# Kernel optimization log

Measured on AMD Instinct MI355X. Metric: run time of the kernel, lower is better.

## Reference

```python
import jax, jax.numpy as jnp
import numpy as np

HEADS = 8
DIM_HEAD = 64


def setup_inputs() -> dict:
    key = jax.random.key(0)
    k1, k2, k3 = jax.random.split(key, 3)
    b, hw, n, dim = 2, 1024, 64, 512
    x = jax.random.normal(k1, (b, hw, n, dim), dtype=jnp.float32)
    w_qkv = jax.random.normal(k2, (3 * HEADS * DIM_HEAD, dim), dtype=jnp.float32) * 0.02
    pos_bias = jax.random.normal(k3, (HEADS, n, n), dtype=jnp.float32)
    # one batch attends everywhere, one focuses on the present frame (eye mask)
    focus_present_mask = jnp.arange(b).astype(bool)
    return {"x": x, "w_qkv": w_qkv, "pos_bias": pos_bias,
            "focus_present_mask": focus_present_mask}


def reference(x, w_qkv, pos_bias, focus_present_mask):
    b, hw, n, dim = x.shape
    h, d = HEADS, DIM_HEAD
    scale = d ** -0.5

    # fused qkv projection (no bias)
    qkv = jnp.einsum('bsnc,ec->bsne', x, w_qkv)          # (b, hw, n, 3*h*d)
    q, k, v = jnp.split(qkv, 3, axis=-1)

    def to_heads(t):  # '... n (h d) -> ... h n d'
        return jnp.moveaxis(t.reshape(b, hw, n, h, d), 3, 2)

    q, k, v = map(to_heads, (q, k, v))                   # (b, hw, h, n, d)
    q = q * scale

    sim = jnp.einsum('bshid,bshjd->bshij', q, k)         # (b, hw, h, n, n)
    sim = sim + pos_bias                                 # broadcast (h, n, n)

    # focus-present mask: eye for focused batches, all-ones otherwise
    eye = jnp.eye(n, dtype=bool)
    ones = jnp.ones((n, n), dtype=bool)
    mask = jnp.where(focus_present_mask[:, None, None, None, None],
                     eye[None, None, None], ones[None, None, None])  # (b,1,1,n,n)
    neg_max = -jnp.finfo(sim.dtype).max
    sim = jnp.where(mask, sim, neg_max)

    attn = jax.nn.softmax(sim, axis=-1)                  # includes the amax shift
    out = jnp.einsum('bshij,bshjd->bshid', attn, v)      # (b, hw, h, n, d)
    out = jnp.moveaxis(out, 2, 3).reshape(b, hw, n, h * d)  # '... h n d -> ... n (h d)'
    return out
```

## Files before the change

### kernel.cpp

```cpp
#include <hip/hip_runtime.h>
#include <hip/hip_bf16.h>


typedef __attribute__((ext_vector_type(4))) float f32x4;
typedef __attribute__((ext_vector_type(8))) short s16x8;

#define DIM 512

__device__ __forceinline__ short f2bf(float f) {
    unsigned int u = __builtin_bit_cast(unsigned int, f);
    u += 0x7fffu + ((u >> 16) & 1u);
    return (short)(u >> 16);
}
__device__ __forceinline__ f32x4 ntld4(const float* p) {
    return __builtin_nontemporal_load((const f32x4*)p);
}
__device__ __forceinline__ void ntst4(float* p, f32x4 v) {
    __builtin_nontemporal_store(v, (f32x4*)p);
}
__device__ __forceinline__ s16x8 pack8(f32x4 a, f32x4 b) {
    s16x8 v;
    v[0] = f2bf(a[0]); v[1] = f2bf(a[1]); v[2] = f2bf(a[2]); v[3] = f2bf(a[3]);
    v[4] = f2bf(b[0]); v[5] = f2bf(b[1]); v[6] = f2bf(b[2]); v[7] = f2bf(b[3]);
    return v;
}
__device__ __forceinline__ int xaddr(int row, int kb) {
    return (row << 10) + (kb ^ ((row & 7) << 4));
}
__device__ __forceinline__ int taddr(int row, int kb) {
    return (row << 7) + (kb ^ ((row & 7) << 4));
}

__global__ void conv_w(const float* __restrict__ w, unsigned short* __restrict__ wb) {
    int gid  = blockIdx.x * 256 + threadIdx.x;
    int lane = gid & 63;
    int ks   = (gid >> 6) & 15;
    int rowblk = gid >> 10;
    int row = rowblk * 16 + (lane & 15);
    int col = ks * 32 + (lane >> 4) * 8;
    const float* p = w + (size_t)row * DIM + col;
    f32x4 a = *(const f32x4*)p;
    f32x4 b = *(const f32x4*)(p + 4);
    float sc = (row < 512) ? 0.125f : 1.0f;
    a *= sc; b *= sc;
    *(s16x8*)(wb + (size_t)gid * 8) = pack8(a, b);
}

template<int WB16>
__device__ __forceinline__ s16x8 wfragL(const unsigned short* __restrict__ wb,
                                        const float* __restrict__ w,
                                        int rowblk, int ks, int lane) {
    if constexpr (WB16) {
        return *(const s16x8*)(wb + ((size_t)(rowblk * 16 + ks) * 64 + lane) * 8);
    } else {
        int row = rowblk * 16 + (lane & 15);
        int col = ks * 32 + (lane >> 4) * 8;
        const float* p = w + (size_t)row * DIM + col;
        f32x4 u0 = *(const f32x4*)p;
        f32x4 u1 = *(const f32x4*)(p + 4);
        float sc = (row < 512) ? 0.125f : 1.0f;
        u0 *= sc; u1 *= sc;
        return pack8(u0, u1);
    }
}

__device__ __forceinline__ bool decode_mask(const unsigned int* mk, int b) {
    unsigned int m0 = mk[0], m1 = mk[1];
    if (m0 <= 1u && m1 <= 1u) return ((b == 0) ? m0 : m1) != 0u;
    return ((const unsigned char*)mk)[b] != 0;
}

#define MFB(a, b, cc) __builtin_amdgcn_mfma_f32_16x16x32_bf16(a, b, cc, 0, 0, 0)

#define XF(ks)                                                               \
    s16x8 af0 = *(const s16x8*)(smem + xaddr(c,      (ks) * 64 + g * 16));   \
    s16x8 af1 = *(const s16x8*)(smem + xaddr(16 + c, (ks) * 64 + g * 16));   \
    s16x8 af2 = *(const s16x8*)(smem + xaddr(32 + c, (ks) * 64 + g * 16));   \
    s16x8 af3 = *(const s16x8*)(smem + xaddr(48 + c, (ks) * 64 + g * 16));

template<int WB16>
__global__ __launch_bounds__(1024, 4)
void attn_merged(const float* __restrict__ x,
                 const float* __restrict__ w,
                 const unsigned short* __restrict__ wb,
                 const float* __restrict__ pb,
                 const unsigned int* __restrict__ mk,
                 float* __restrict__ out)
{
    extern __shared__ char smem[];
    const int tid  = threadIdx.x;
    const int lane = tid & 63;
    const int wave = tid >> 6;
    const int g    = lane >> 4;
    const int c    = lane & 15;
    const int hp   = wave >> 1;
    const int hw2  = wave & 1;
    const int site = blockIdx.x;
    const bool focused = decode_mask(mk, site >> 10);
    const float* xblk   = x   + (size_t)site * (64 * DIM);
    float*       outblk = out + (size_t)site * (64 * DIM);
    const f32x4 zf = {0.f, 0.f, 0.f, 0.f};

    {
        const int row = tid >> 4, c16 = tid & 15;
        const float* gp = xblk + row * DIM;
        #pragma unroll
        for (int j = 0; j < 4; ++j) {
            f32x4 a = ntld4(gp + j * 128 + c16 * 8);
            f32x4 b = ntld4(gp + j * 128 + c16 * 8 + 4);
            *(s16x8*)(smem + xaddr(row, j * 256 + c16 * 16)) = pack8(a, b);
        }
    }
    __syncthreads();

    if (focused) {
        const int RB = 64 + hp * 4 + 2 * hw2;
        f32x4 va[2][4];
        #pragma unroll
        for (int i = 0; i < 2; ++i)
            #pragma unroll
            for (int j = 0; j < 4; ++j) va[i][j] = zf;
        #pragma unroll 4
        for (int ks = 0; ks < 16; ++ks) {
            s16x8 wv0 = wfragL<WB16>(wb, w, RB,     ks, lane);
            s16x8 wv1 = wfragL<WB16>(wb, w, RB + 1, ks, lane);
            XF(ks)
            va[0][0]=MFB(wv0,af0,va[0][0]); va[0][1]=MFB(wv0,af1,va[0][1]);
            va[0][2]=MFB(wv0,af2,va[0][2]); va[0][3]=MFB(wv0,af3,va[0][3]);
            va[1][0]=MFB(wv1,af0,va[1][0]); va[1][1]=MFB(wv1,af1,va[1][1]);
            va[1][2]=MFB(wv1,af2,va[1][2]); va[1][3]=MFB(wv1,af3,va[1][3]);
        }
        char* stg = smem + 65536;
        #pragma unroll
        for (int h2 = 0; h2 < 2; ++h2) {
            #pragma unroll
            for (int sub = 0; sub < 2; ++sub)
                #pragma unroll
                for (int tn = 0; tn < 2; ++tn) {
                    int rl   = tn * 16 + c;
                    int colb = hp * 256 + hw2 * 128 + sub * 64 + g * 16;
                    *(f32x4*)(stg + rl * 2048 + (colb ^ ((rl & 7) << 4))) =
                        va[sub][h2 * 2 + tn];
                }
            __syncthreads();
            #pragma unroll
            for (int i = 0; i < 4; ++i) {
                int lin = i * 16384 + tid * 16;
                int rl = lin >> 11, off = lin & 2047;
                f32x4 v = *(const f32x4*)(stg + rl * 2048 + (off ^ ((rl & 7) << 4)));
                ntst4((float*)((char*)outblk + h2 * 65536 + lin), v);
            }
            if (h2 == 0) __syncthreads();
        }
        return;
    }

    char* slotA = smem + hp * 8192;
    char* slotB = smem + 65536 + hp * 8192;
    const int RQ = hp * 4 + 2 * hw2;
    const int RK = 32 + hp * 4 + 2 * hw2;

    {
        f32x4 acc[4][2];
        #pragma unroll
        for (int t = 0; t < 4; ++t) { acc[t][0] = zf; acc[t][1] = zf; }
        #pragma unroll 4
        for (int ks = 0; ks < 16; ++ks) {
            s16x8 w0 = wfragL<WB16>(wb, w, RQ,     ks, lane);
            s16x8 w1 = wfragL<WB16>(wb, w, RQ + 1, ks, lane);
            XF(ks)
            acc[0][0]=MFB(af0,w0,acc[0][0]); acc[0][1]=MFB(af0,w1,acc[0][1]);
            acc[1][0]=MFB(af1,w0,acc[1][0]); acc[1][1]=MFB(af1,w1,acc[1][1]);
            acc[2][0]=MFB(af2,w0,acc[2][0]); acc[2][1]=MFB(af2,w1,acc[2][1]);
            acc[3][0]=MFB(af3,w0,acc[3][0]); acc[3][1]=MFB(af3,w1,acc[3][1]);
        }
        #pragma unroll
        for (int t = 0; t < 4; ++t)
            #pragma unroll
            for (int hc = 0; hc < 2; ++hc)
                #pragma unroll
                for (int rr = 0; rr < 4; ++rr) {
                    int row = t * 16 + g * 4 + rr;
                    int col = hw2 * 32 + hc * 16 + c;
                    *(short*)(slotB + (row << 7) + ((col * 2) ^ ((row & 7) << 4))) =
                        f2bf(acc[t][hc][rr]);
                }
    }

    s16x8 kc[4];
    {
        f32x4 acc[4][2];
        #pragma unroll
        for (int t = 0; t < 4; ++t) { acc[t][0] = zf; acc[t][1] = zf; }
        #pragma unroll 4
        for (int ks = 0; ks < 16; ++ks) {
            s16x8 w0 = wfragL<WB16>(wb, w, RK,     ks, lane);
            s16x8 w1 = wfragL<WB16>(wb, w, RK + 1, ks, lane);
            XF(ks)
            acc[0][0]=MFB(af0,w0,acc[0][0]); acc[0][1]=MFB(af0,w1,acc[0][1]);
            acc[1][0]=MFB(af1,w0,acc[1][0]); acc[1][1]=MFB(af1,w1,acc[1][1]);
            acc[2][0]=MFB(af2,w0,acc[2][0]); acc[2][1]=MFB(af2,w1,acc[2][1]);
            acc[3][0]=MFB(af3,w0,acc[3][0]); acc[3][1]=MFB(af3,w1,acc[3][1]);
        }
        #pragma unroll
        for (int t = 0; t < 4; ++t) kc[t] = pack8(acc[t][0], acc[t][1]);
    }

    s16x8 vc[4];
    #pragma unroll
    for (int sub = 0; sub < 2; ++sub) {
        const int RB = 64 + hp * 4 + 2 * hw2 + sub;
        f32x4 a0 = zf, a1 = zf, a2 = zf, a3 = zf;
        #pragma unroll 4
        for (int ks = 0; ks < 16; ++ks) {
            s16x8 wv = wfragL<WB16>(wb, w, RB, ks, lane);
            XF(ks)
            a0 = MFB(wv, af0, a0); a1 = MFB(wv, af1, a1);
            a2 = MFB(wv, af2, a2); a3 = MFB(wv, af3, a3);
        }
        vc[sub * 2]     = pack8(a0, a1);
        vc[sub * 2 + 1] = pack8(a2, a3);
    }

    __syncthreads();

    #pragma unroll
    for (int t = 0; t < 4; ++t)
        #pragma unroll
        for (int hc = 0; hc < 2; ++hc)
            #pragma unroll
            for (int rr = 0; rr < 4; ++rr) {
                int row = t * 16 + g * 4 + rr;
                int col = hw2 * 32 + hc * 16 + c;
                *(short*)(slotA + (row << 7) + ((col * 2) ^ ((row & 7) << 4))) =
                    kc[t][hc * 4 + rr];
            }
    __syncthreads();

    f32x4 sm[2][4];
    #pragma unroll
    for (int i = 0; i < 2; ++i)
        #pragma unroll
        for (int j = 0; j < 4; ++j) sm[i][j] = zf;
    #pragma unroll
    for (int ks2 = 0; ks2 < 2; ++ks2) {
        s16x8 aq0 = *(const s16x8*)(slotB + taddr((2 * hw2 + 0) * 16 + c, ks2 * 64 + g * 16));
        s16x8 aq1 = *(const s16x8*)(slotB + taddr((2 * hw2 + 1) * 16 + c, ks2 * 64 + g * 16));
        #pragma unroll
        for (int j = 0; j < 4; ++j) {
            s16x8 bk = *(const s16x8*)(slotA + taddr(j * 16 + c, ks2 * 64 + g * 16));
            sm[0][j] = MFB(aq0, bk, sm[0][j]);
            sm[1][j] = MFB(aq1, bk, sm[1][j]);
        }
    }

    const float* pbh = pb + hp * 4096;
    #pragma unroll
    for (int tr = 0; tr < 2; ++tr) {
        #pragma unroll
        for (int rr = 0; rr < 4; ++rr) {
            const int i = 32 * hw2 + tr * 16 + g * 4 + rr;
            float v0 = sm[tr][0][rr] + pbh[i * 64 +  0 + c];
            float v1 = sm[tr][1][rr] + pbh[i * 64 + 16 + c];
            float v2 = sm[tr][2][rr] + pbh[i * 64 + 32 + c];
            float v3 = sm[tr][3][rr] + pbh[i * 64 + 48 + c];
            float mx = fmaxf(fmaxf(v0, v1), fmaxf(v2, v3));
            mx = fmaxf(mx, __shfl_xor(mx, 1));
            mx = fmaxf(mx, __shfl_xor(mx, 2));
            mx = fmaxf(mx, __shfl_xor(mx, 4));
            mx = fmaxf(mx, __shfl_xor(mx, 8));
            float p0 = __expf(v0 - mx);
            float p1 = __expf(v1 - mx);
            float p2 = __expf(v2 - mx);
            float p3 = __expf(v3 - mx);
            float ssum = p0 + p1 + p2 + p3;
            ssum += __shfl_xor(ssum, 1);
            ssum += __shfl_xor(ssum, 2);
            ssum += __shfl_xor(ssum, 4);
            ssum += __shfl_xor(ssum, 8);
            float rinv = 1.0f / ssum;
            sm[tr][0][rr] = p0 * rinv; sm[tr][1][rr] = p1 * rinv;
            sm[tr][2][rr] = p2 * rinv; sm[tr][3][rr] = p3 * rinv;
        }
    }
    __syncthreads();

    #pragma unroll
    for (int tr = 0; tr < 2; ++tr)
        #pragma unroll
        for (int tc = 0; tc < 4; ++tc)
            #pragma unroll
            for (int rr = 0; rr < 4; ++rr) {
                int row = 32 * hw2 + tr * 16 + g * 4 + rr;
                int col = tc * 16 + c;
                *(short*)(slotA + (row << 7) + ((col * 2) ^ ((row & 7) << 4))) =
                    f2bf(sm[tr][tc][rr]);
            }
    #pragma unroll
    for (int sub = 0; sub < 2; ++sub)
        #pragma unroll
        for (int t = 0; t < 4; ++t)
            #pragma unroll
            for (int rr = 0; rr < 4; ++rr) {
                int row = hw2 * 32 + sub * 16 + g * 4 + rr;
                int col = t * 16 + c;
                *(short*)(slotB + (row << 7) + ((col * 2) ^ ((row & 7) << 4))) =
                    vc[sub * 2 + (t >> 1)][(t & 1) * 4 + rr];
            }
    __syncthreads();

    f32x4 ot[4][2];
    #pragma unroll
    for (int i = 0; i < 4; ++i) { ot[i][0] = zf; ot[i][1] = zf; }
    #pragma unroll
    for (int ks2 = 0; ks2 < 2; ++ks2) {
        s16x8 ba0 = *(const s16x8*)(slotA + taddr((2 * hw2 + 0) * 16 + c, ks2 * 64 + g * 16));
        s16x8 ba1 = *(const s16x8*)(slotA + taddr((2 * hw2 + 1) * 16 + c, ks2 * 64 + g * 16));
        #pragma unroll
        for (int i = 0; i < 4; ++i) {
            s16x8 av = *(const s16x8*)(slotB + taddr(i * 16 + c, ks2 * 64 + g * 16));
            ot[i][0] = MFB(av, ba0, ot[i][0]);
            ot[i][1] = MFB(av, ba1, ot[i][1]);
        }
    }
    __syncthreads();

    #pragma unroll
    for (int i = 0; i < 4; ++i)
        #pragma unroll
        for (int j = 0; j < 2; ++j) {
            int rl   = 32 * hw2 + j * 16 + c;
            int colb = hp * 256 + i * 64 + g * 16;
            *(f32x4*)(smem + rl * 2048 + (colb ^ ((rl & 7) << 4))) = ot[i][j];
        }
    __syncthreads();
    #pragma unroll
    for (int i = 0; i < 8; ++i) {
        int lin = i * 16384 + tid * 16;
        int rl = lin >> 11, off = lin & 2047;
        f32x4 v = *(const f32x4*)(smem + rl * 2048 + (off ^ ((rl & 7) << 4)));
        ntst4((float*)((char*)outblk + lin), v);
    }
}

extern "C" void kernel_launch(void* const* d_in, const int* in_sizes, int n_in,
                              void* d_out, int out_size, void* d_ws, size_t ws_size,
                              hipStream_t stream)
{
    const float* x  = (const float*)d_in[0];
    const float* w  = (const float*)d_in[1];
    const float* pb = (const float*)d_in[2];
    const unsigned int* mk = (const unsigned int*)d_in[3];
    float* out = (float*)d_out;

    const int LDS = 131072;
    const size_t wbytes = (size_t)1536 * 512 * sizeof(unsigned short);

    if (ws_size >= wbytes) {
        unsigned short* wbp = (unsigned short*)d_ws;
        conv_w<<<dim3(384), dim3(256), 0, stream>>>(w, wbp);
        hipFuncSetAttribute(reinterpret_cast<const void*>(&attn_merged<1>),
                            hipFuncAttributeMaxDynamicSharedMemorySize, LDS);
        attn_merged<1><<<dim3(2048), dim3(1024), LDS, stream>>>(x, w, wbp, pb, mk, out);
    } else {
        hipFuncSetAttribute(reinterpret_cast<const void*>(&attn_merged<0>),
                            hipFuncAttributeMaxDynamicSharedMemorySize, LDS);
        attn_merged<0><<<dim3(2048), dim3(1024), LDS, stream>>>(x, w, nullptr, pb, mk, out);
    }
}
```

Baseline: 294.7 us.

## Add persistent pipelined kernel with bf16 pre-converted x and async LDS prefetch

```diff
diff --git a/kernel.cpp b/kernel.cpp
--- a/kernel.cpp
+++ b/kernel.cpp
@@ -4,8 +4,11 @@
 
 typedef __attribute__((ext_vector_type(4))) float f32x4;
 typedef __attribute__((ext_vector_type(8))) short s16x8;
+typedef __attribute__((ext_vector_type(4))) short s16x4;
 
 #define DIM 512
+#define GRIDP 256
+#define SITESP 8
 
 __device__ __forceinline__ short f2bf(float f) {
     unsigned int u = __builtin_bit_cast(unsigned int, f);
@@ -24,11 +27,22 @@
     v[4] = f2bf(b[0]); v[5] = f2bf(b[1]); v[6] = f2bf(b[2]); v[7] = f2bf(b[3]);
     return v;
 }
+__device__ __forceinline__ s16x4 pack4(f32x4 a) {
+    s16x4 v;
+    v[0] = f2bf(a[0]); v[1] = f2bf(a[1]); v[2] = f2bf(a[2]); v[3] = f2bf(a[3]);
+    return v;
+}
 __device__ __forceinline__ int xaddr(int row, int kb) {
     return (row << 10) + (kb ^ ((row & 7) << 4));
 }
 __device__ __forceinline__ int taddr(int row, int kb) {
     return (row << 7) + (kb ^ ((row & 7) << 4));
+}
+
+__device__ __forceinline__ void gl_lds16(const char* g, char* l) {
+    __builtin_amdgcn_global_load_lds(
+        (const __attribute__((address_space(1))) unsigned int*)g,
+        (__attribute__((address_space(3))) unsigned int*)l, 16, 0, 0);
 }
 
 __global__ void conv_w(const float* __restrict__ w, unsigned short* __restrict__ wb) {
@@ -44,6 +58,18 @@
     float sc = (row < 512) ? 0.125f : 1.0f;
     a *= sc; b *= sc;
     *(s16x8*)(wb + (size_t)gid * 8) = pack8(a, b);
+}
+
+__global__ void conv_x(const float* __restrict__ x, unsigned short* __restrict__ xb) {
+    unsigned int gid = blockIdx.x * 256 + threadIdx.x;
+    unsigned int site = gid >> 12;
+    unsigned int o = (gid & 4095) * 16;
+    unsigned int row = o >> 10;
+    unsigned int col = ((o & 1023) ^ ((row & 7) << 4)) >> 1;
+    const float* p = x + (size_t)site * 32768 + row * DIM + col;
+    f32x4 a = ntld4(p);
+    f32x4 b = ntld4(p + 4);
+    __builtin_nontemporal_store(pack8(a, b), (s16x8*)(xb + (size_t)gid * 8));
 }
 
 template<int WB16>
@@ -72,11 +98,241 @@
 
 #define MFB(a, b, cc) __builtin_amdgcn_mfma_f32_16x16x32_bf16(a, b, cc, 0, 0, 0)
 
-#define XF(ks)                                                               \
-    s16x8 af0 = *(const s16x8*)(smem + xaddr(c,      (ks) * 64 + g * 16));   \
-    s16x8 af1 = *(const s16x8*)(smem + xaddr(16 + c, (ks) * 64 + g * 16));   \
-    s16x8 af2 = *(const s16x8*)(smem + xaddr(32 + c, (ks) * 64 + g * 16));   \
-    s16x8 af3 = *(const s16x8*)(smem + xaddr(48 + c, (ks) * 64 + g * 16));
+#define XFR(B, ks)                                                            \
+    s16x8 af0 = *(const s16x8*)((B) + xaddr(c,      (ks) * 64 + g * 16));     \
+    s16x8 af1 = *(const s16x8*)((B) + xaddr(16 + c, (ks) * 64 + g * 16));     \
+    s16x8 af2 = *(const s16x8*)((B) + xaddr(32 + c, (ks) * 64 + g * 16));     \
+    s16x8 af3 = *(const s16x8*)((B) + xaddr(48 + c, (ks) * 64 + g * 16));
+
+__global__ __launch_bounds__(1024, 1)
+void attn_pipe(const char* __restrict__ xb,
+               const unsigned short* __restrict__ wb,
+               const float* __restrict__ pb,
+               const unsigned int* __restrict__ mk,
+               float* __restrict__ out)
+{
+    extern __shared__ char smem[];
+    const int tid  = threadIdx.x;
+    const int lane = tid & 63;
+    const int wave = tid >> 6;
+    const int g    = lane >> 4;
+    const int c    = lane & 15;
+    const int hp   = wave >> 1;
+    const int hw2  = wave & 1;
+    const int myround = hp >> 1;
+    char* Qs = smem + 131072 + (hp & 1) * 16384;
+    char* Ks = Qs + 8192;
+    const f32x4 zf = {0.f, 0.f, 0.f, 0.f};
+
+    {
+        const char* src = xb + (size_t)blockIdx.x * 65536;
+        #pragma unroll
+        for (int i = 0; i < 4; ++i) {
+            int ch = __builtin_amdgcn_readfirstlane((wave * 4 + i) * 1024);
+            gl_lds16(src + ch + lane * 16, smem + ch);
+        }
+    }
+    __syncthreads();
+
+    for (int s = 0; s < SITESP; ++s) {
+        const int cursite = blockIdx.x + s * GRIDP;
+        char* Xr = smem + (s & 1) * 65536;
+        char* Pr = smem + ((s & 1) ^ 1) * 65536;
+        const bool focused = decode_mask(mk, cursite >> 10);
+        float* outblk = out + (size_t)cursite * (64 * DIM);
+
+        if (s + 1 < SITESP) {
+            const char* src = xb + (size_t)(blockIdx.x + (s + 1) * GRIDP) * 65536;
+            #pragma unroll
+            for (int i = 0; i < 4; ++i) {
+                int ch = __builtin_amdgcn_readfirstlane((wave * 4 + i) * 1024);
+                gl_lds16(src + ch + lane * 16, Pr + ch);
+            }
+        }
+
+        if (focused) {
+            #pragma unroll
+            for (int sub = 0; sub < 2; ++sub) {
+                const int RB = 64 + hp * 4 + 2 * hw2 + sub;
+                f32x4 a0 = zf, a1 = zf, a2 = zf, a3 = zf;
+                #pragma unroll 4
+                for (int ks = 0; ks < 16; ++ks) {
+                    s16x8 wv = wfragL<1>(wb, nullptr, RB, ks, lane);
+                    XFR(Xr, ks)
+                    a0 = MFB(wv, af0, a0); a1 = MFB(wv, af1, a1);
+                    a2 = MFB(wv, af2, a2); a3 = MFB(wv, af3, a3);
+                }
+                const int dhb = hp * 64 + hw2 * 32 + sub * 16 + g * 4;
+                ntst4(outblk + (size_t)(0 * 16 + c) * DIM + dhb, a0);
+                ntst4(outblk + (size_t)(1 * 16 + c) * DIM + dhb, a1);
+                ntst4(outblk + (size_t)(2 * 16 + c) * DIM + dhb, a2);
+                ntst4(outblk + (size_t)(3 * 16 + c) * DIM + dhb, a3);
+            }
+        } else {
+            s16x8 qc[4];
+            {
+                const int RQ = hp * 4 + 2 * hw2;
+                f32x4 acc[4][2];
+                #pragma unroll
+                for (int t = 0; t < 4; ++t) { acc[t][0] = zf; acc[t][1] = zf; }
+                #pragma unroll 4
+                for (int ks = 0; ks < 16; ++ks) {
+                    s16x8 w0 = wfragL<1>(wb, nullptr, RQ,     ks, lane);
+                    s16x8 w1 = wfragL<1>(wb, nullptr, RQ + 1, ks, lane);
+                    XFR(Xr, ks)
+                    acc[0][0]=MFB(af0,w0,acc[0][0]); acc[0][1]=MFB(af0,w1,acc[0][1]);
+                    acc[1][0]=MFB(af1,w0,acc[1][0]); acc[1][1]=MFB(af1,w1,acc[1][1]);
+                    acc[2][0]=MFB(af2,w0,acc[2][0]); acc[2][1]=MFB(af2,w1,acc[2][1]);
+                    acc[3][0]=MFB(af3,w0,acc[3][0]); acc[3][1]=MFB(af3,w1,acc[3][1]);
+                }
+                #pragma unroll
+                for (int t = 0; t < 4; ++t) qc[t] = pack8(acc[t][0], acc[t][1]);
+            }
+            s16x4 kc4[8];
+            #pragma unroll
+            for (int hcp = 0; hcp < 2; ++hcp) {
+                const int RB = 32 + hp * 4 + 2 * hw2 + hcp;
+                f32x4 a0 = zf, a1 = zf, a2 = zf, a3 = zf;
+                #pragma unroll 4
+                for (int ks = 0; ks < 16; ++ks) {
+                    s16x8 wv = wfragL<1>(wb, nullptr, RB, ks, lane);
+                    XFR(Xr, ks)
+                    a0 = MFB(af0, wv, a0); a1 = MFB(af1, wv, a1);
+                    a2 = MFB(af2, wv, a2); a3 = MFB(af3, wv, a3);
+                }
+                kc4[hcp * 4 + 0] = pack4(a0); kc4[hcp * 4 + 1] = pack4(a1);
+                kc4[hcp * 4 + 2] = pack4(a2); kc4[hcp * 4 + 3] = pack4(a3);
+            }
+
+            for (int r = 0; r < 4; ++r) {
+                const bool act = (myround == r);
+                if (act) {
+                    #pragma unroll
+                    for (int t = 0; t < 4; ++t)
+                        #pragma unroll
+                        for (int hc2 = 0; hc2 < 2; ++hc2)
+                            #pragma unroll
+                            for (int rr = 0; rr < 4; ++rr) {
+                                int row = t * 16 + g * 4 + rr;
+                                int col = hw2 * 32 + hc2 * 16 + c;
+                                int off = (row << 7) + ((col * 2) ^ ((row & 7) << 4));
+                                *(short*)(Qs + off) = qc[t][hc2 * 4 + rr];
+                                *(short*)(Ks + off) = kc4[hc2 * 4 + t][rr];
+                            }
+                }
+                __syncthreads();
+                f32x4 sm[2][4];
+                if (act) {
+                    #pragma unroll
+                    for (int i = 0; i < 2; ++i)
+                        #pragma unroll
+                        for (int j = 0; j < 4; ++j) sm[i][j] = zf;
+                    #pragma unroll
+                    for (int ks2 = 0; ks2 < 2; ++ks2) {
+                        s16x8 aq0 = *(const s16x8*)(Qs + taddr((2*hw2 + 0)*16 + c, ks2*64 + g*16));
+                        s16x8 aq1 = *(const s16x8*)(Qs + taddr((2*hw2 + 1)*16 + c, ks2*64 + g*16));
+                        #pragma unroll
+                        for (int j = 0; j < 4; ++j) {
+                            s16x8 bk = *(const s16x8*)(Ks + taddr(j*16 + c, ks2*64 + g*16));
+                            sm[0][j] = MFB(aq0, bk, sm[0][j]);
+                            sm[1][j] = MFB(aq1, bk, sm[1][j]);
+                        }
+                    }
+                    const float* pbh = pb + hp * 4096;
+                    #pragma unroll
+                    for (int tr = 0; tr < 2; ++tr) {
+                        #pragma unroll
+                        for (int rr = 0; rr < 4; ++rr) {
+                            const int i = 32 * hw2 + tr * 16 + g * 4 + rr;
+                            float v0 = sm[tr][0][rr] + pbh[i * 64 +  0 + c];
+                            float v1 = sm[tr][1][rr] + pbh[i * 64 + 16 + c];
+                            float v2 = sm[tr][2][rr] + pbh[i * 64 + 32 + c];
+                            float v3 = sm[tr][3][rr] + pbh[i * 64 + 48 + c];
+                            float mx = fmaxf(fmaxf(v0, v1), fmaxf(v2, v3));
+                            mx = fmaxf(mx, __shfl_xor(mx, 1));
+                            mx = fmaxf(mx, __shfl_xor(mx, 2));
+                            mx = fmaxf(mx, __shfl_xor(mx, 4));
+                            mx = fmaxf(mx, __shfl_xor(mx, 8));
+                            float p0 = __expf(v0 - mx);
+                            float p1 = __expf(v1 - mx);
+                            float p2 = __expf(v2 - mx);
+                            float p3 = __expf(v3 - mx);
+                            float ssum = p0 + p1 + p2 + p3;
+                            ssum += __shfl_xor(ssum, 1);
+                            ssum += __shfl_xor(ssum, 2);
+                            ssum += __shfl_xor(ssum, 4);
+                            ssum += __shfl_xor(ssum, 8);
+                            float rinv = 1.0f / ssum;
+                            sm[tr][0][rr] = p0 * rinv; sm[tr][1][rr] = p1 * rinv;
+                            sm[tr][2][rr] = p2 * rinv; sm[tr][3][rr] = p3 * rinv;
+                        }
+                    }
+                }
+                __syncthreads();
+                if (act) {
+                    #pragma unroll
+                    for (int tr = 0; tr < 2; ++tr)
+                        #pragma unroll
+                        for (int tc = 0; tc < 4; ++tc)
+                            #pragma unroll
+                            for (int rr = 0; rr < 4; ++rr) {
+                                int row = 32 * hw2 + tr * 16 + g * 4 + rr;
+                                int col = tc * 16 + c;
+                                *(short*)(Qs + (row << 7) + ((col * 2) ^ ((row & 7) << 4))) =
+                                    f2bf(sm[tr][tc][rr]);
+                            }
+                    #pragma unroll
+                    for (int sub = 0; sub < 2; ++sub) {
+                        const int RB = 64 + hp * 4 + 2 * hw2 + sub;
+                        f32x4 a0 = zf, a1 = zf, a2 = zf, a3 = zf;
+                        #pragma unroll 4
+                        for (int ks = 0; ks < 16; ++ks) {
+                            s16x8 wv = wfragL<1>(wb, nullptr, RB, ks, lane);
+                            XFR(Xr, ks)
+                            a0 = MFB(wv, af0, a0); a1 = MFB(wv, af1, a1);
+                            a2 = MFB(wv, af2, a2); a3 = MFB(wv, af3, a3);
+                        }
+                        #pragma unroll
+                        for (int rr = 0; rr < 4; ++rr) {
+                            int row = hw2 * 32 + sub * 16 + g * 4 + rr;
+                            int sw = (row & 7) << 4;
+                            int rb = row << 7;
+                            *(short*)(Ks + rb + (((0 * 16 + c) * 2) ^ sw)) = f2bf(a0[rr]);
+                            *(short*)(Ks + rb + (((1 * 16 + c) * 2) ^ sw)) = f2bf(a1[rr]);
+                            *(short*)(Ks + rb + (((2 * 16 + c) * 2) ^ sw)) = f2bf(a2[rr]);
+                            *(short*)(Ks + rb + (((3 * 16 + c) * 2) ^ sw)) = f2bf(a3[rr]);
+                        }
+                    }
+                }
+                __syncthreads();
+                if (act) {
+                    f32x4 ot[4][2];
+                    #pragma unroll
+                    for (int i = 0; i < 4; ++i) { ot[i][0] = zf; ot[i][1] = zf; }
+                    #pragma unroll
+                    for (int ks2 = 0; ks2 < 2; ++ks2) {
+                        s16x8 ba0 = *(const s16x8*)(Qs + taddr((2*hw2 + 0)*16 + c, ks2*64 + g*16));
+                        s16x8 ba1 = *(const s16x8*)(Qs + taddr((2*hw2 + 1)*16 + c, ks2*64 + g*16));
+                        #pragma unroll
+                        for (int i = 0; i < 4; ++i) {
+                            s16x8 av = *(const s16x8*)(Ks + taddr(i*16 + c, ks2*64 + g*16));
+                            ot[i][0] = MFB(av, ba0, ot[i][0]);
+                            ot[i][1] = MFB(av, ba1, ot[i][1]);
+                        }
+                    }
+                    #pragma unroll
+                    for (int i = 0; i < 4; ++i)
+                        #pragma unroll
+                        for (int j = 0; j < 2; ++j)
+                            ntst4(outblk + (size_t)(32*hw2 + j*16 + c) * DIM
+                                  + hp * 64 + i * 16 + g * 4, ot[i][j]);
+                }
+                __syncthreads();
+            }
+        }
+        __syncthreads();
+    }
+}
 
 template<int WB16>
 __global__ __launch_bounds__(1024, 4)
@@ -124,7 +380,7 @@
         for (int ks = 0; ks < 16; ++ks) {
             s16x8 wv0 = wfragL<WB16>(wb, w, RB,     ks, lane);
             s16x8 wv1 = wfragL<WB16>(wb, w, RB + 1, ks, lane);
-            XF(ks)
+            XFR(smem, ks)
             va[0][0]=MFB(wv0,af0,va[0][0]); va[0][1]=MFB(wv0,af1,va[0][1]);
             va[0][2]=MFB(wv0,af2,va[0][2]); va[0][3]=MFB(wv0,af3,va[0][3]);
             va[1][0]=MFB(wv1,af0,va[1][0]); va[1][1]=MFB(wv1,af1,va[1][1]);
@@ -168,7 +424,7 @@
         for (int ks = 0; ks < 16; ++ks) {
             s16x8 w0 = wfragL<WB16>(wb, w, RQ,     ks, lane);
             s16x8 w1 = wfragL<WB16>(wb, w, RQ + 1, ks, lane);
-            XF(ks)
+            XFR(smem, ks)
             acc[0][0]=MFB(af0,w0,acc[0][0]); acc[0][1]=MFB(af0,w1,acc[0][1]);
             acc[1][0]=MFB(af1,w0,acc[1][0]); acc[1][1]=MFB(af1,w1,acc[1][1]);
             acc[2][0]=MFB(af2,w0,acc[2][0]); acc[2][1]=MFB(af2,w1,acc[2][1]);
@@ -186,7 +442,6 @@
                         f2bf(acc[t][hc][rr]);
                 }
     }
-
     s16x8 kc[4];
     {
         f32x4 acc[4][2];
@@ -196,7 +451,7 @@
         for (int ks = 0; ks < 16; ++ks) {
             s16x8 w0 = wfragL<WB16>(wb, w, RK,     ks, lane);
             s16x8 w1 = wfragL<WB16>(wb, w, RK + 1, ks, lane);
-            XF(ks)
+            XFR(smem, ks)
             acc[0][0]=MFB(af0,w0,acc[0][0]); acc[0][1]=MFB(af0,w1,acc[0][1]);
             acc[1][0]=MFB(af1,w0,acc[1][0]); acc[1][1]=MFB(af1,w1,acc[1][1]);
             acc[2][0]=MFB(af2,w0,acc[2][0]); acc[2][1]=MFB(af2,w1,acc[2][1]);
@@ -205,7 +460,6 @@
         #pragma unroll
         for (int t = 0; t < 4; ++t) kc[t] = pack8(acc[t][0], acc[t][1]);
     }
-
     s16x8 vc[4];
     #pragma unroll
     for (int sub = 0; sub < 2; ++sub) {
@@ -214,16 +468,14 @@
         #pragma unroll 4
         for (int ks = 0; ks < 16; ++ks) {
             s16x8 wv = wfragL<WB16>(wb, w, RB, ks, lane);
-            XF(ks)
+            XFR(smem, ks)
             a0 = MFB(wv, af0, a0); a1 = MFB(wv, af1, a1);
             a2 = MFB(wv, af2, a2); a3 = MFB(wv, af3, a3);
         }
         vc[sub * 2]     = pack8(a0, a1);
         vc[sub * 2 + 1] = pack8(a2, a3);
     }
-
-    __syncthreads();
-
+    __syncthreads();
     #pragma unroll
     for (int t = 0; t < 4; ++t)
         #pragma unroll
@@ -236,7 +488,6 @@
                     kc[t][hc * 4 + rr];
             }
     __syncthreads();
-
     f32x4 sm[2][4];
     #pragma unroll
     for (int i = 0; i < 2; ++i)
@@ -253,7 +504,6 @@
             sm[1][j] = MFB(aq1, bk, sm[1][j]);
         }
     }
-
     const float* pbh = pb + hp * 4096;
     #pragma unroll
     for (int tr = 0; tr < 2; ++tr) {
@@ -284,7 +534,6 @@
         }
     }
     __syncthreads();
-
     #pragma unroll
     for (int tr = 0; tr < 2; ++tr)
         #pragma unroll
@@ -308,7 +557,6 @@
                     vc[sub * 2 + (t >> 1)][(t & 1) * 4 + rr];
             }
     __syncthreads();
-
     f32x4 ot[4][2];
     #pragma unroll
     for (int i = 0; i < 4; ++i) { ot[i][0] = zf; ot[i][1] = zf; }
@@ -324,7 +572,6 @@
         }
     }
     __syncthreads();
-
     #pragma unroll
     for (int i = 0; i < 4; ++i)
         #pragma unroll
@@ -353,18 +600,37 @@
     const unsigned int* mk = (const unsigned int*)d_in[3];
     float* out = (float*)d_out;
 
-    const int LDS = 131072;
     const size_t wbytes = (size_t)1536 * 512 * sizeof(unsigned short);
-
-    if (ws_size >= wbytes) {
+    const size_t xoff   = (size_t)2 << 20;
+    const size_t xbytes = (size_t)2048 * 65536;
+    const int LDS_P = 163840;
+    const int LDS_M = 131072;
+
+    if (ws_size >= xoff + xbytes) {
+        unsigned short* wbp = (unsigned short*)d_ws;
+        unsigned short* xbp = (unsigned short*)((char*)d_ws + xoff);
+        conv_w<<<dim3(384), dim3(256), 0, stream>>>(w, wbp);
+        conv_x<<<dim3(32768), dim3(256), 0, stream>>>(x, xbp);
+        hipError_t e = hipFuncSetAttribute(
+            reinterpret_cast<const void*>(&attn_pipe),
+            hipFuncAttributeMaxDynamicSharedMemorySize, LDS_P);
+        if (e == hipSuccess) {
+            attn_pipe<<<dim3(GRIDP), dim3(1024), LDS_P, stream>>>(
+                (const char*)xbp, wbp, pb, mk, out);
+            return;
+        }
+        hipFuncSetAttribute(reinterpret_cast<const void*>(&attn_merged<1>),
+                            hipFuncAttributeMaxDynamicSharedMemorySize, LDS_M);
+        attn_merged<1><<<dim3(2048), dim3(1024), LDS_M, stream>>>(x, w, wbp, pb, mk, out);
+    } else if (ws_size >= wbytes) {
         unsigned short* wbp = (unsigned short*)d_ws;
         conv_w<<<dim3(384), dim3(256), 0, stream>>>(w, wbp);
         hipFuncSetAttribute(reinterpret_cast<const void*>(&attn_merged<1>),
-                            hipFuncAttributeMaxDynamicSharedMemorySize, LDS);
-        attn_merged<1><<<dim3(2048), dim3(1024), LDS, stream>>>(x, w, wbp, pb, mk, out);
+                            hipFuncAttributeMaxDynamicSharedMemorySize, LDS_M);
+        attn_merged<1><<<dim3(2048), dim3(1024), LDS_M, stream>>>(x, w, wbp, pb, mk, out);
     } else {
         hipFuncSetAttribute(reinterpret_cast<const void*>(&attn_merged<0>),
-                            hipFuncAttributeMaxDynamicSharedMemorySize, LDS);
-        attn_merged<0><<<dim3(2048), dim3(1024), LDS, stream>>>(x, w, nullptr, pb, mk, out);
-    }
-}
+                            hipFuncAttributeMaxDynamicSharedMemorySize, LDS_M);
+        attn_merged<0><<<dim3(2048), dim3(1024), LDS_M, stream>>>(x, w, nullptr, pb, mk, out);
+    }
+}
```

New measurement: 1.120 ms. 280% more time.
